# Kernel optimization log

Measured on AMD Instinct MI355X. Metric: run time of the kernel, lower is better.

Reference implementation:

```python
import jax, jax.numpy as jnp
import numpy as np

L = 2048        # sequence length
D_INNER = 2048  # d_inner; must equal d_state for the original scan to typecheck
D_STATE = 2048
DT_RANK = 16
D_CONV = 4
DT_SCALE = 1.0


def setup_inputs() -> dict:
    key = jax.random.key(0)
    ks = jax.random.split(key, 4)
    return {
        "x": jax.random.normal(ks[0], (L, D_INNER), jnp.float32),
        # dt_proj: Dense(dt_rank) -> W:(D_INNER, DT_RANK), b:(DT_RANK,) (lecun-normal-ish scale)
        "dt_W": jax.random.normal(ks[1], (D_INNER, DT_RANK), jnp.float32) / np.sqrt(D_INNER).astype(np.float32),
        "dt_b": jnp.zeros((DT_RANK,), jnp.float32),
        # flax nn.Conv kernel layout: (window, in_features, out_features) == WIO
        "conv_kernel": jax.random.normal(ks[2], (D_CONV, D_INNER, D_INNER), jnp.float32) / np.sqrt(D_CONV * D_INNER).astype(np.float32),
        "conv_b": jnp.zeros((D_INNER,), jnp.float32),
        "A_param": 0.02 * jax.random.normal(ks[3], (D_STATE, D_INNER), jnp.float32),
        "D_param": jnp.ones((D_INNER,), jnp.float32),
    }


@jax.jit
def _fwd(x, dt_W, dt_b, conv_kernel, conv_b, A_param, D_param):
    # dt branch: computed exactly as in the original module, but (as in the
    # original) its result is never consumed downstream.
    dt = jax.nn.softplus(x @ dt_W + dt_b) * DT_SCALE  # noqa: F841 (faithful dead code)

    # conv1d over the sequence dim, SAME padding (lo=1, hi=2 for k=4)
    xc = jax.lax.conv_general_dilated(
        x[None],                      # (1, L, D_INNER)
        conv_kernel,                  # (D_CONV, D_INNER, D_INNER)
        window_strides=(1,),
        padding="SAME",
        dimension_numbers=("NWC", "WIO", "NWC"),
    )[0] + conv_b                     # (L, D_INNER)

    A = -jnp.exp(A_param)             # (D_STATE, D_INNER) == (D_INNER, D_INNER)

    # Faithful scan: carry = A @ carry + x_t, per-step output is x_t itself,
    # so the scan's ys are exactly xc (the carry is discarded).
    def step(carry, xt):
        return A @ carry + xt, xt

    _, y = jax.lax.scan(step, jnp.zeros((D_INNER,), x.dtype), xc)
    return y * D_param


def reference(x, dt_W, dt_b, conv_kernel, conv_b, A_param, D_param):
    return _fwd(x, dt_W, dt_b, conv_kernel, conv_b, A_param, D_param)
```

## Files before the change

### kernel.cpp

```cpp
#include <hip/hip_runtime.h>
#include <hip/hip_bf16.h>
#include <stdint.h>

#define L_SEQ 2048
#define DI    2048
#define KTOT  8192
#define BM 128
#define BN 128
#define BK 64
#define KSTEPS (2048 / BK)
#define XPAD_ROWS 2052

typedef __attribute__((ext_vector_type(4))) float f32x4;
typedef __attribute__((ext_vector_type(8))) short bf16x8;

__device__ __forceinline__ unsigned short f2bf(float f) {
  union { float f; unsigned u; } v; v.f = f;
  unsigned r = v.u + 0x7FFFu + ((v.u >> 16) & 1u);
  return (unsigned short)(r >> 16);
}

__global__ void prep_xpad(const float* __restrict__ x,
                          unsigned short* __restrict__ xpad) {
  const long e = ((long)blockIdx.x * blockDim.x + threadIdx.x) * 4;
  const int row = (int)(e >> 11);
  const int col = (int)(e & 2047);
  ushort4 o;
  if (row >= 1 && row <= L_SEQ) {
    const float4 v = *(const float4*)(x + (long)(row - 1) * DI + col);
    o.x = f2bf(v.x); o.y = f2bf(v.y); o.z = f2bf(v.z); o.w = f2bf(v.w);
  } else {
    o.x = 0; o.y = 0; o.z = 0; o.w = 0;
  }
  *(ushort4*)(xpad + e) = o;
}

__global__ __launch_bounds__(256) void prep_bt(const float* __restrict__ ck,
                                               unsigned short* __restrict__ bt) {
  __shared__ float tile[64][65];
  const int w  = blockIdx.z;
  const int i0 = blockIdx.x * 64;
  const int n0 = blockIdx.y * 64;
  const int t  = threadIdx.x;
  const float* src = ck + ((long)w * 2048 + i0) * DI + n0;
#pragma unroll
  for (int r = 0; r < 4; ++r) {
    const int row = r * 16 + (t >> 4);
    const int c4  = (t & 15) * 4;
    const float4 v = *(const float4*)(src + (long)row * DI + c4);
    tile[row][c4 + 0] = v.x;
    tile[row][c4 + 1] = v.y;
    tile[row][c4 + 2] = v.z;
    tile[row][c4 + 3] = v.w;
  }
  __syncthreads();
#pragma unroll
  for (int j2 = 0; j2 < 2; ++j2) {
    const int n  = (t >> 3) + j2 * 32;
    const int ic = (t & 7) * 8;
    union { unsigned short u[8]; uint4 v; } o;
#pragma unroll
    for (int j = 0; j < 8; ++j) o.u[j] = f2bf(tile[ic + j][n]);
    *(uint4*)(bt + (long)(n0 + n) * KTOT + (long)w * 2048 + i0 + ic) = o.v;
  }
}

__global__ __launch_bounds__(256, 4) void gemm_conv(
    const unsigned short* __restrict__ xpad,
    const unsigned short* __restrict__ bt,
    const float* __restrict__ bias,
    const float* __restrict__ dscale,
    float* __restrict__ out) {
  __shared__ unsigned short As[BM * BK];
  __shared__ unsigned short Bs[BN * BK];

  const int tid  = threadIdx.x;
  const int bm   = blockIdx.x >> 4;
  const int bn   = blockIdx.x & 15;
  const int w    = blockIdx.y;
  const int lane = tid & 63;
  const int wid  = tid >> 6;
  const int wr   = wid >> 1;
  const int wc   = wid & 1;

  const int sm0 = tid >> 3;
  const int sk  = (tid & 7) * 8;

  f32x4 acc[4][4];
#pragma unroll
  for (int i = 0; i < 4; ++i)
#pragma unroll
    for (int j = 0; j < 4; ++j)
      acc[i][j] = (f32x4){0.f, 0.f, 0.f, 0.f};

  const int fm = lane & 15;
  const int kq = (lane >> 4) * 8;

  const unsigned short* gA0 = xpad + (long)(bm * BM + sm0 + w) * DI + sk;
  const unsigned short* gB0 = bt + (long)(bn * BN + sm0) * KTOT + (long)w * 2048 + sk;
  unsigned short* lA = &As[tid * 8];
  unsigned short* lB = &Bs[tid * 8];

  for (int kt = 0; kt < KSTEPS; ++kt) {
    const unsigned short* gA = gA0 + kt * BK;
    const unsigned short* gB = gB0 + kt * BK;
#pragma unroll
    for (int r = 0; r < 4; ++r) {
      __builtin_amdgcn_global_load_lds(
          (const __attribute__((address_space(1))) void*)(gA + (long)r * 32 * DI),
          (__attribute__((address_space(3))) void*)(lA + r * 2048), 16, 0, 0);
      __builtin_amdgcn_global_load_lds(
          (const __attribute__((address_space(1))) void*)(gB + (long)r * 32 * KTOT),
          (__attribute__((address_space(3))) void*)(lB + r * 2048), 16, 0, 0);
    }
    __syncthreads();
#pragma unroll
    for (int s = 0; s < 2; ++s) {
      bf16x8 av[4], bv[4];
#pragma unroll
      for (int f = 0; f < 4; ++f)
        av[f] = *(const bf16x8*)&As[(wr * 64 + f * 16 + fm) * BK + s * 32 + kq];
#pragma unroll
      for (int f = 0; f < 4; ++f)
        bv[f] = *(const bf16x8*)&Bs[(wc * 64 + f * 16 + fm) * BK + s * 32 + kq];
#pragma unroll
      for (int i = 0; i < 4; ++i)
#pragma unroll
        for (int j = 0; j < 4; ++j)
          acc[i][j] = __builtin_amdgcn_mfma_f32_16x16x32_bf16(av[i], bv[j],
                                                              acc[i][j], 0, 0, 0);
    }
    __syncthreads();
  }

  const int r0 = bm * BM + wr * 64;
  const int c0 = bn * BN + wc * 64;
#pragma unroll
  for (int j = 0; j < 4; ++j) {
    const int col = c0 + j * 16 + fm;
    const float bb = (w == 0) ? bias[col] : 0.f;
    const float dd = dscale[col];
#pragma unroll
    for (int i = 0; i < 4; ++i) {
      const int row = r0 + i * 16 + (lane >> 4) * 4;
#pragma unroll
      for (int q = 0; q < 4; ++q)
        atomicAdd(&out[(long)(row + q) * DI + col], (acc[i][j][q] + bb) * dd);
    }
  }
}

extern "C" void kernel_launch(void* const* d_in, const int* in_sizes, int n_in,
                              void* d_out, int out_size, void* d_ws, size_t ws_size,
                              hipStream_t stream) {
  const float* x  = (const float*)d_in[0];
  const float* ck = (const float*)d_in[3];
  const float* cb = (const float*)d_in[4];
  const float* Dp = (const float*)d_in[6];
  float* out = (float*)d_out;

  unsigned short* xpad = (unsigned short*)d_ws;
  unsigned short* Bt =
      (unsigned short*)((char*)d_ws + (size_t)XPAD_ROWS * DI * sizeof(unsigned short));

  prep_xpad<<<(XPAD_ROWS * DI) / (4 * 256), 256, 0, stream>>>(x, xpad);
  prep_bt<<<dim3(32, 32, 4), 256, 0, stream>>>(ck, Bt);
  hipMemsetAsync(d_out, 0, (size_t)out_size * sizeof(float), stream);
  gemm_conv<<<dim3(16 * 16, 4), 256, 0, stream>>>(xpad, Bt, cb, Dp, out);
}
```

Measured before the change: 248.5 us.

## Double-buffer LDS tiles in conv GEMM and remap blocks for XCD locality

Adds a two-stage LDS ping-pong so the global-to-LDS loads for the next K tile are issued while MFMAs run on the current tile, which removes one barrier per iteration. Loads all fragments up front and raises wave priority around the MFMA burst. It also flattens the grid and remaps block IDs so consecutive blocks on the same XCD share operand tiles, aiming at better L2 reuse. LDS use doubles to 64 KB per block and launch bounds drop to 2 blocks per SIMD group, which lowers occupancy.

After: 269.7 us. +8.6%, slower.

```diff
diff --git a/kernel.cpp b/kernel.cpp
--- a/kernel.cpp
+++ b/kernel.cpp
@@ -65,19 +65,21 @@
   }
 }
 
-__global__ __launch_bounds__(256, 4) void gemm_conv(
+__global__ __launch_bounds__(256, 2) void gemm_conv(
     const unsigned short* __restrict__ xpad,
     const unsigned short* __restrict__ bt,
     const float* __restrict__ bias,
     const float* __restrict__ dscale,
     float* __restrict__ out) {
-  __shared__ unsigned short As[BM * BK];
-  __shared__ unsigned short Bs[BN * BK];
+  __shared__ unsigned short As[2][BM * BK];
+  __shared__ unsigned short Bs[2][BN * BK];
+
+  const int logical = (blockIdx.x & 7) * 128 + (blockIdx.x >> 3);
+  const int w  = logical >> 8;
+  const int bm = (logical >> 4) & 15;
+  const int bn = logical & 15;
 
   const int tid  = threadIdx.x;
-  const int bm   = blockIdx.x >> 4;
-  const int bn   = blockIdx.x & 15;
-  const int w    = blockIdx.y;
   const int lane = tid & 63;
   const int wid  = tid >> 6;
   const int wr   = wid >> 1;
@@ -98,12 +100,12 @@
 
   const unsigned short* gA0 = xpad + (long)(bm * BM + sm0 + w) * DI + sk;
   const unsigned short* gB0 = bt + (long)(bn * BN + sm0) * KTOT + (long)w * 2048 + sk;
-  unsigned short* lA = &As[tid * 8];
-  unsigned short* lB = &Bs[tid * 8];
 
-  for (int kt = 0; kt < KSTEPS; ++kt) {
+  auto stage = [&](int buf, int kt) {
     const unsigned short* gA = gA0 + kt * BK;
     const unsigned short* gB = gB0 + kt * BK;
+    unsigned short* lA = &As[buf][tid * 8];
+    unsigned short* lB = &Bs[buf][tid * 8];
 #pragma unroll
     for (int r = 0; r < 4; ++r) {
       __builtin_amdgcn_global_load_lds(
@@ -113,24 +115,36 @@
           (const __attribute__((address_space(1))) void*)(gB + (long)r * 32 * KTOT),
           (__attribute__((address_space(3))) void*)(lB + r * 2048), 16, 0, 0);
     }
-    __syncthreads();
+  };
+
+  stage(0, 0);
+  __syncthreads();
+
+  int cur = 0;
+  for (int kt = 0; kt < KSTEPS; ++kt) {
+    if (kt + 1 < KSTEPS) stage(cur ^ 1, kt + 1);
+    const unsigned short* Ac = &As[cur][0];
+    const unsigned short* Bc = &Bs[cur][0];
+    bf16x8 av[2][4], bv[2][4];
 #pragma unroll
-    for (int s = 0; s < 2; ++s) {
-      bf16x8 av[4], bv[4];
+    for (int s = 0; s < 2; ++s)
 #pragma unroll
-      for (int f = 0; f < 4; ++f)
-        av[f] = *(const bf16x8*)&As[(wr * 64 + f * 16 + fm) * BK + s * 32 + kq];
+      for (int f = 0; f < 4; ++f) {
+        av[s][f] = *(const bf16x8*)&Ac[(wr * 64 + f * 16 + fm) * BK + s * 32 + kq];
+        bv[s][f] = *(const bf16x8*)&Bc[(wc * 64 + f * 16 + fm) * BK + s * 32 + kq];
+      }
+    __builtin_amdgcn_s_setprio(1);
 #pragma unroll
-      for (int f = 0; f < 4; ++f)
-        bv[f] = *(const bf16x8*)&Bs[(wc * 64 + f * 16 + fm) * BK + s * 32 + kq];
+    for (int s = 0; s < 2; ++s)
 #pragma unroll
       for (int i = 0; i < 4; ++i)
 #pragma unroll
         for (int j = 0; j < 4; ++j)
-          acc[i][j] = __builtin_amdgcn_mfma_f32_16x16x32_bf16(av[i], bv[j],
+          acc[i][j] = __builtin_amdgcn_mfma_f32_16x16x32_bf16(av[s][i], bv[s][j],
                                                               acc[i][j], 0, 0, 0);
-    }
+    __builtin_amdgcn_s_setprio(0);
     __syncthreads();
+    cur ^= 1;
   }
 
   const int r0 = bm * BM + wr * 64;
@@ -166,5 +180,5 @@
   prep_xpad<<<(XPAD_ROWS * DI) / (4 * 256), 256, 0, stream>>>(x, xpad);
   prep_bt<<<dim3(32, 32, 4), 256, 0, stream>>>(ck, Bt);
   hipMemsetAsync(d_out, 0, (size_t)out_size * sizeof(float), stream);
-  gemm_conv<<<dim3(16 * 16, 4), 256, 0, stream>>>(xpad, Bt, cb, Dp, out);
+  gemm_conv<<<16 * 16 * 4, 256, 0, stream>>>(xpad, Bt, cb, Dp, out);
 }
```

## Enlarge GEMM tiles to 256x256 with double-buffered swizzled LDS pipeline

Applied to the files above, without the earlier changes.

Rewrites the conv-as-GEMM kernel to use 256x256 output tiles with 512 threads and 8 waves, each wave holding an 8x4 MFMA accumulator block. LDS is double-buffered so the next K-slice is fetched while the current one is consumed. An XOR swizzle on K chunks avoids LDS bank conflicts, and the block index is remapped to group tiles. The aim is more data reuse per byte loaded and latency hiding, at the cost of higher register and LDS pressure (128KB LDS) and fewer blocks (256).

Result: no change. 247.6 us (-0.4%).

```diff
diff --git a/kernel.cpp b/kernel.cpp
--- a/kernel.cpp
+++ b/kernel.cpp
@@ -5,14 +5,16 @@
 #define L_SEQ 2048
 #define DI    2048
 #define KTOT  8192
-#define BM 128
-#define BN 128
-#define BK 64
-#define KSTEPS (2048 / BK)
+#define TM    256
+#define TK    64
+#define NTILE 32
 #define XPAD_ROWS 2052
 
 typedef __attribute__((ext_vector_type(4))) float f32x4;
 typedef __attribute__((ext_vector_type(8))) short bf16x8;
+
+#define AS1 __attribute__((address_space(1)))
+#define AS3 __attribute__((address_space(3)))
 
 __device__ __forceinline__ unsigned short f2bf(float f) {
   union { float f; unsigned u; } v; v.f = f;
@@ -65,87 +67,126 @@
   }
 }
 
-__global__ __launch_bounds__(256, 4) void gemm_conv(
+__global__ __launch_bounds__(512, 2) void gemm_conv(
     const unsigned short* __restrict__ xpad,
     const unsigned short* __restrict__ bt,
     const float* __restrict__ bias,
     const float* __restrict__ dscale,
     float* __restrict__ out) {
-  __shared__ unsigned short As[BM * BK];
-  __shared__ unsigned short Bs[BN * BK];
+  __shared__ unsigned short lds[2][2][TM * TK];
 
   const int tid  = threadIdx.x;
-  const int bm   = blockIdx.x >> 4;
-  const int bn   = blockIdx.x & 15;
-  const int w    = blockIdx.y;
   const int lane = tid & 63;
-  const int wid  = tid >> 6;
-  const int wr   = wid >> 1;
-  const int wc   = wid & 1;
-
-  const int sm0 = tid >> 3;
-  const int sk  = (tid & 7) * 8;
-
-  f32x4 acc[4][4];
-#pragma unroll
-  for (int i = 0; i < 4; ++i)
-#pragma unroll
-    for (int j = 0; j < 4; ++j)
-      acc[i][j] = (f32x4){0.f, 0.f, 0.f, 0.f};
-
-  const int fm = lane & 15;
-  const int kq = (lane >> 4) * 8;
-
-  const unsigned short* gA0 = xpad + (long)(bm * BM + sm0 + w) * DI + sk;
-  const unsigned short* gB0 = bt + (long)(bn * BN + sm0) * KTOT + (long)w * 2048 + sk;
-  unsigned short* lA = &As[tid * 8];
-  unsigned short* lB = &Bs[tid * 8];
-
-  for (int kt = 0; kt < KSTEPS; ++kt) {
-    const unsigned short* gA = gA0 + kt * BK;
-    const unsigned short* gB = gB0 + kt * BK;
+  const int wave = tid >> 6;
+  const int wr   = wave >> 2;
+  const int wc   = wave & 3;
+  const int fm   = lane & 15;
+  const int g    = lane >> 4;
+
+  const int l  = ((int)blockIdx.x & 7) * 32 + ((int)blockIdx.x >> 3);
+  const int w  = l >> 6;
+  const int bm = (l >> 3) & 7;
+  const int bn = l & 7;
+
+  const long rowA0 = (long)bm * TM + w;
+  const long colB0 = (long)bn * TM;
+  const long wk    = (long)w * 2048;
+
+  const int baseA = (wr * 128 + fm) * 128;
+  const int baseB = (wc * 64 + fm) * 128;
+  int xorb[2];
+  xorb[0] = ((0 + g) ^ (fm & 7)) * 16;
+  xorb[1] = ((4 + g) ^ (fm & 7)) * 16;
+
+  f32x4 acc[8][4];
+#pragma unroll
+  for (int m = 0; m < 8; ++m)
+#pragma unroll
+    for (int n = 0; n < 4; ++n)
+      acc[m][n] = (f32x4){0.f, 0.f, 0.f, 0.f};
+
+  auto stageT = [&](int buf, int kt) {
+    const long kb = (long)kt * TK;
+    unsigned short* lA = &lds[buf][0][0];
+    unsigned short* lB = &lds[buf][1][0];
 #pragma unroll
     for (int r = 0; r < 4; ++r) {
-      __builtin_amdgcn_global_load_lds(
-          (const __attribute__((address_space(1))) void*)(gA + (long)r * 32 * DI),
-          (__attribute__((address_space(3))) void*)(lA + r * 2048), 16, 0, 0);
-      __builtin_amdgcn_global_load_lds(
-          (const __attribute__((address_space(1))) void*)(gB + (long)r * 32 * KTOT),
-          (__attribute__((address_space(3))) void*)(lB + r * 2048), 16, 0, 0);
-    }
-    __syncthreads();
-#pragma unroll
-    for (int s = 0; s < 2; ++s) {
-      bf16x8 av[4], bv[4];
-#pragma unroll
-      for (int f = 0; f < 4; ++f)
-        av[f] = *(const bf16x8*)&As[(wr * 64 + f * 16 + fm) * BK + s * 32 + kq];
-#pragma unroll
-      for (int f = 0; f < 4; ++f)
-        bv[f] = *(const bf16x8*)&Bs[(wc * 64 + f * 16 + fm) * BK + s * 32 + kq];
-#pragma unroll
-      for (int i = 0; i < 4; ++i)
-#pragma unroll
-        for (int j = 0; j < 4; ++j)
-          acc[i][j] = __builtin_amdgcn_mfma_f32_16x16x32_bf16(av[i], bv[j],
-                                                              acc[i][j], 0, 0, 0);
-    }
-    __syncthreads();
-  }
-
-  const int r0 = bm * BM + wr * 64;
-  const int c0 = bn * BN + wc * 64;
-#pragma unroll
-  for (int j = 0; j < 4; ++j) {
-    const int col = c0 + j * 16 + fm;
-    const float bb = (w == 0) ? bias[col] : 0.f;
-    const float dd = dscale[col];
-#pragma unroll
-    for (int i = 0; i < 4; ++i) {
-      const int row = r0 + i * 16 + (lane >> 4) * 4;
-#pragma unroll
-      for (int q = 0; q < 4; ++q)
-        atomicAdd(&out[(long)(row + q) * DI + col], (acc[i][j][q] + bb) * dd);
+      const int s   = r * 512 + tid;
+      const int row = s >> 3;
+      const int k0  = (s & 7) ^ (row & 7);
+      const unsigned short* gA = xpad + (rowA0 + row) * DI + kb + k0 * 8;
+      __builtin_amdgcn_global_load_lds((const AS1 void*)gA,
+                                       (AS3 void*)(lA + (size_t)s * 8), 16, 0, 0);
+      const unsigned short* gB = bt + (colB0 + row) * KTOT + wk + kb + k0 * 8;
+      __builtin_amdgcn_global_load_lds((const AS1 void*)gB,
+                                       (AS3 void*)(lB + (size_t)s * 8), 16, 0, 0);
+    }
+  };
+
+  auto consume = [&](int buf) {
+    const char* Ab = (const char*)&lds[buf][0][0];
+    const char* Bb = (const char*)&lds[buf][1][0];
+    bf16x8 bv[4][2];
+#pragma unroll
+    for (int q = 0; q < 4; ++q) {
+      bf16x8 av[2][2];
+      if (q == 0) {
+#pragma unroll
+        for (int n = 0; n < 4; ++n)
+#pragma unroll
+          for (int s = 0; s < 2; ++s)
+            bv[n][s] = *(const bf16x8*)(Bb + baseB + n * 2048 + xorb[s]);
+      }
+#pragma unroll
+      for (int mm = 0; mm < 2; ++mm)
+#pragma unroll
+        for (int s = 0; s < 2; ++s)
+          av[mm][s] = *(const bf16x8*)(Ab + baseA + (q * 2 + mm) * 2048 + xorb[s]);
+      __builtin_amdgcn_s_barrier();
+      asm volatile("s_waitcnt lgkmcnt(0)" ::: "memory");
+      __builtin_amdgcn_sched_barrier(0);
+      __builtin_amdgcn_s_setprio(1);
+#pragma unroll
+      for (int s = 0; s < 2; ++s)
+#pragma unroll
+        for (int mm = 0; mm < 2; ++mm)
+#pragma unroll
+          for (int n = 0; n < 4; ++n)
+            acc[q * 2 + mm][n] = __builtin_amdgcn_mfma_f32_16x16x32_bf16(
+                av[mm][s], bv[n][s], acc[q * 2 + mm][n], 0, 0, 0);
+      __builtin_amdgcn_s_setprio(0);
+      __builtin_amdgcn_sched_barrier(0);
+      __builtin_amdgcn_s_barrier();
+    }
+  };
+
+  stageT(0, 0);
+  for (int it = 0; it < 16; ++it) {
+    stageT(1, 2 * it + 1);
+    asm volatile("s_waitcnt vmcnt(8)" ::: "memory");
+    __builtin_amdgcn_s_barrier();
+    consume(0);
+    if (it < 15) {
+      stageT(0, 2 * it + 2);
+      asm volatile("s_waitcnt vmcnt(8)" ::: "memory");
+    } else {
+      asm volatile("s_waitcnt vmcnt(0)" ::: "memory");
+    }
+    __builtin_amdgcn_s_barrier();
+    consume(1);
+  }
+
+#pragma unroll
+  for (int m = 0; m < 8; ++m) {
+    const long row = (long)bm * TM + wr * 128 + m * 16 + g * 4;
+#pragma unroll
+    for (int n = 0; n < 4; ++n) {
+      const int col = bn * TM + wc * 64 + n * 16 + fm;
+      const float bb = (w == 0) ? bias[col] : 0.f;
+      const float dd = dscale[col];
+#pragma unroll
+      for (int qq = 0; qq < 4; ++qq)
+        atomicAdd(&out[(row + qq) * DI + col], (acc[m][n][qq] + bb) * dd);
     }
   }
 }
@@ -166,5 +207,5 @@
   prep_xpad<<<(XPAD_ROWS * DI) / (4 * 256), 256, 0, stream>>>(x, xpad);
   prep_bt<<<dim3(32, 32, 4), 256, 0, stream>>>(ck, Bt);
   hipMemsetAsync(d_out, 0, (size_t)out_size * sizeof(float), stream);
-  gemm_conv<<<dim3(16 * 16, 4), 256, 0, stream>>>(xpad, Bt, cb, Dp, out);
-}
+  gemm_conv<<<8 * 8 * 4, 512, 0, stream>>>(xpad, Bt, cb, Dp, out);
+}
```
